# Optimization experiments

Measured on AMD Instinct MI355X. Metric: run time of the kernel, lower is better.

The kernel has to match this reference:

```python
import jax, jax.numpy as jnp
import numpy as np

N_NODES = 100000


def setup_inputs() -> dict:
    key = jax.random.key(0)
    k1, k2, k3, k4, k5 = jax.random.split(key, 5)
    feat = jax.random.normal(k1, (N_NODES, 128), dtype=jnp.float32)
    src = jax.random.randint(k2, (1600000,), 0, N_NODES, dtype=jnp.int32)
    dst = jax.random.randint(k3, (1600000,), 0, N_NODES, dtype=jnp.int32)
    # Xavier-uniform-like weight init
    limit = float(np.sqrt(6.0 / (128 + 128)))
    weight = jax.random.uniform(k4, (128, 128), minval=-limit, maxval=limit, dtype=jnp.float32)
    bias = jax.random.normal(k5, (128,), dtype=jnp.float32) * 0.0  # zeros per reset_parameters
    return {"feat": feat, "src": src, "dst": dst, "weight": weight, "bias": bias}


def reference(feat, src, dst, weight, bias):
    # copy_u/sum: gather source features along edges, scatter-add into destinations
    agg = jax.ops.segment_sum(feat[src], dst, num_segments=N_NODES)  # [N, in_feats]
    rst = agg @ weight  # [N, out_feats]
    # symmetric-ish degree normalization: in_degree^{-0.5}, clamped at 1
    deg = jax.ops.segment_sum(jnp.ones_like(dst, dtype=feat.dtype), dst, num_segments=N_NODES)
    norm = jnp.clip(deg, 1.0, None) ** -0.5  # [N]
    rst = rst * norm[:, None] + bias
    return rst
```

## Files before the change

kernel.cpp:

```cpp
#include <hip/hip_runtime.h>
#include <hip/hip_bf16.h>

#define CHUNK 1024
#define RR 64
#define DEPTH 64
#define WMAX 1600
typedef unsigned int uint;
typedef unsigned short ushort;

typedef __bf16 bf16x8 __attribute__((ext_vector_type(8)));
typedef float  f32x4  __attribute__((ext_vector_type(4)));

__device__ __forceinline__ ushort f2bf(float f) {
    const uint u = __float_as_uint(f);
    return (ushort)((u + 0x7fffu + ((u >> 16) & 1u)) >> 16);
}

__global__ __launch_bounds__(256) void partition64(const int* __restrict__ src,
                                                   const int* __restrict__ dst,
                                                   int* __restrict__ gcur,
                                                   int2* __restrict__ staging,
                                                   int cap, int nE, int N) {
    __shared__ int2 bins[RR][DEPTH];
    __shared__ int cnt[RR];
    __shared__ int res[RR];
    const int t  = threadIdx.x;
    const int nb = gridDim.x;
    const int rounds = (nE + nb * 1024 - 1) / (nb * 1024);

    for (int rd = 0; rd < rounds; ++rd) {
        if (t < RR) cnt[t] = 0;
        __syncthreads();

        const int e4 = (rd * nb + blockIdx.x) * 1024 + t * 4;
        int s[4], d[4];
        int nv = 0;
        if (e4 + 3 < nE) {
            const int4 s4 = *reinterpret_cast<const int4*>(src + e4);
            const int4 d4 = *reinterpret_cast<const int4*>(dst + e4);
            s[0] = s4.x; s[1] = s4.y; s[2] = s4.z; s[3] = s4.w;
            d[0] = d4.x; d[1] = d4.y; d[2] = d4.z; d[3] = d4.w;
            nv = 4;
        } else {
            for (int e = e4; e < nE; ++e) { s[nv] = src[e]; d[nv] = dst[e]; ++nv; }
        }
#pragma unroll
        for (int i = 0; i < 4; ++i) {
            if (i < nv) {
                const int r = (int)(((long long)d[i] * RR) / N);
                const int pos = atomicAdd(&cnt[r], 1);
                if (pos < DEPTH) {
                    bins[r][pos] = make_int2(s[i], d[i]);
                } else {
                    const int gp = atomicAdd(&gcur[r], 1);
                    staging[(size_t)r * cap + gp] = make_int2(s[i], d[i]);
                }
            }
        }
        __syncthreads();
        if (t < RR) {
            int c = cnt[t];
            c = c < DEPTH ? c : DEPTH;
            cnt[t] = c;
            res[t] = (c > 0) ? atomicAdd(&gcur[t], c) : 0;
        }
        __syncthreads();
        {
            const int g = t >> 2;
            const int l = t & 3;
            const int c = cnt[g];
            const int b = res[g];
            for (int i = l; i < c; i += 4)
                staging[(size_t)g * cap + b + i] = bins[g][i];
        }
        __syncthreads();
    }
}

__global__ __launch_bounds__(1024) void range_build(const int2* __restrict__ staging,
                                                    const int* __restrict__ gcur,
                                                    int* __restrict__ deg,
                                                    int* __restrict__ off,
                                                    int* __restrict__ csr,
                                                    int cap, int N) {
    __shared__ int hist[WMAX];
    __shared__ int sbuf[1024];
    __shared__ int sbase;
    const int r = blockIdx.x;
    const int t = threadIdx.x;
    const int lo = (int)(((long long)r * N + RR - 1) / RR);
    const int hi = (int)(((long long)(r + 1) * N + RR - 1) / RR);
    const int W  = hi - lo;
    const int cnt = gcur[r];

    if (t < RR) sbuf[t] = gcur[t];
    for (int i = t; i < W; i += 1024) hist[i] = 0;
    __syncthreads();
    if (t == 0) {
        int b = 0;
        for (int i = 0; i < r; ++i) b += sbuf[i];
        sbase = b;
    }
    const int2* ep = staging + (size_t)r * cap;
    for (int i = t; i < cnt; i += 1024) {
        const int2 p = ep[i];
        atomicAdd(&hist[p.y - lo], 1);
    }
    __syncthreads();
    const int base = sbase;

    const int i0 = t * 2, i1 = t * 2 + 1;
    const int a = (i0 < W) ? hist[i0] : 0;
    const int b = (i1 < W) ? hist[i1] : 0;
    if (i0 < W) deg[lo + i0] = a;
    if (i1 < W) deg[lo + i1] = b;
    const int tsum = a + b;
    sbuf[t] = tsum;
    __syncthreads();
    for (int dd = 1; dd < 1024; dd <<= 1) {
        const int x = (t >= dd) ? sbuf[t - dd] : 0;
        __syncthreads();
        sbuf[t] += x;
        __syncthreads();
    }
    const int excl = sbuf[t] - tsum;
    if (i0 < W) { off[lo + i0] = base + excl;     hist[i0] = base + excl; }
    if (i1 < W) { off[lo + i1] = base + excl + a; hist[i1] = base + excl + a; }
    __syncthreads();

    for (int i = t; i < cnt; i += 1024) {
        const int2 p = ep[i];
        const int pos = atomicAdd(&hist[p.y - lo], 1);
        csr[pos] = p.x;
    }
}

__global__ __launch_bounds__(256) void prep_w(const float* __restrict__ w,
                                              ushort* __restrict__ wt) {
    const int idx = blockIdx.x * 256 + threadIdx.x;
    const int k = idx >> 7;
    const int n = idx & 127;
    wt[n * 128 + k] = f2bf(w[k * 128 + n]);
}

#define APITCH 136
__global__ __launch_bounds__(256, 2) void gemm_mfma(const float* __restrict__ feat,
                                                    const ushort* __restrict__ wt,
                                                    ushort* __restrict__ h, int M) {
    __shared__ ushort A_lds[64 * APITCH];
    const int t    = threadIdx.x;
    const int wave = t >> 6;
    const int lane = t & 63;
    const int quad = lane >> 4;
    const int nn   = lane & 15;
    const int row0 = blockIdx.x * 64;

    union UB { uint4 u; bf16x8 b; };
    UB bfrag[8][4];
#pragma unroll
    for (int ct = 0; ct < 8; ++ct)
#pragma unroll
        for (int kc = 0; kc < 4; ++kc)
            bfrag[ct][kc].u = *reinterpret_cast<const uint4*>(
                wt + (ct * 16 + nn) * 128 + kc * 32 + quad * 8);

#pragma unroll
    for (int p = 0; p < 8; ++p) {
        const int idx = p * 256 + t;
        const int row = idx >> 5;
        const int c4  = (idx & 31) * 4;
        const int grow = row0 + row;
        float4 v = make_float4(0.f, 0.f, 0.f, 0.f);
        if (grow < M)
            v = *reinterpret_cast<const float4*>(&feat[(size_t)grow * 128 + c4]);
        const uint2 pk = make_uint2((uint)f2bf(v.x) | ((uint)f2bf(v.y) << 16),
                                    (uint)f2bf(v.z) | ((uint)f2bf(v.w) << 16));
        *reinterpret_cast<uint2*>(&A_lds[row * APITCH + c4]) = pk;
    }
    __syncthreads();

    union UA { uint4 u; bf16x8 b; };
    UA afrag[4];
#pragma unroll
    for (int kc = 0; kc < 4; ++kc)
        afrag[kc].u = *reinterpret_cast<const uint4*>(
            &A_lds[(wave * 16 + nn) * APITCH + kc * 32 + quad * 8]);

    f32x4 acc[8];
#pragma unroll
    for (int ct = 0; ct < 8; ++ct) {
        acc[ct] = (f32x4){0.f, 0.f, 0.f, 0.f};
#pragma unroll
        for (int kc = 0; kc < 4; ++kc)
            acc[ct] = __builtin_amdgcn_mfma_f32_16x16x32_bf16(
                afrag[kc].b, bfrag[ct][kc].b, acc[ct], 0, 0, 0);
    }
    __syncthreads();

#pragma unroll
    for (int ct = 0; ct < 8; ++ct) {
#pragma unroll
        for (int reg = 0; reg < 4; ++reg) {
            const int rl = wave * 16 + quad * 4 + reg;
            A_lds[rl * APITCH + ct * 16 + nn] = f2bf(acc[ct][reg]);
        }
    }
    __syncthreads();

#pragma unroll
    for (int p = 0; p < 4; ++p) {
        const int idx = p * 256 + t;
        const int row = idx >> 4;
        const int c16 = idx & 15;
        const int grow = row0 + row;
        if (grow < M) {
            const uint4 v = *reinterpret_cast<const uint4*>(&A_lds[row * APITCH + c16 * 8]);
            *reinterpret_cast<uint4*>(&h[(size_t)grow * 128 + c16 * 8]) = v;
        }
    }
}

__global__ __launch_bounds__(256) void aggregate_h(const ushort* __restrict__ h,
                                                   const int* __restrict__ csr,
                                                   const int* __restrict__ off,
                                                   const int* __restrict__ deg,
                                                   const float* __restrict__ bias,
                                                   float* __restrict__ out, int N) {
    const int node = (blockIdx.x * blockDim.x + threadIdx.x) >> 6;
    if (node >= N) return;
    const int lane = threadIdx.x & 63;
    const int q   = lane >> 4;
    const int sub = lane & 15;
    const int start = off[node];
    const int cnt   = deg[node];
    const int end   = start + cnt;

    float acc[8];
#pragma unroll
    for (int k = 0; k < 8; ++k) acc[k] = 0.0f;

#define UNPACK_ADD(rr)                                             \
    do {                                                           \
        acc[0] += __uint_as_float(((rr).x & 0xffffu) << 16);       \
        acc[1] += __uint_as_float((rr).x & 0xffff0000u);           \
        acc[2] += __uint_as_float(((rr).y & 0xffffu) << 16);       \
        acc[3] += __uint_as_float((rr).y & 0xffff0000u);           \
        acc[4] += __uint_as_float(((rr).z & 0xffffu) << 16);       \
        acc[5] += __uint_as_float((rr).z & 0xffff0000u);           \
        acc[6] += __uint_as_float(((rr).w & 0xffffu) << 16);       \
        acc[7] += __uint_as_float((rr).w & 0xffff0000u);           \
    } while (0)

    int j = start;
    for (; j + 15 < end; j += 16) {
        int s[4];
#pragma unroll
        for (int k = 0; k < 4; ++k) s[k] = csr[j + q + 4 * k];
        uint4 r[4];
#pragma unroll
        for (int k = 0; k < 4; ++k)
            r[k] = *reinterpret_cast<const uint4*>(h + (size_t)s[k] * 128 + sub * 8);
#pragma unroll
        for (int k = 0; k < 4; ++k) UNPACK_ADD(r[k]);
    }
    for (; j + 3 < end; j += 4) {
        const int s = csr[j + q];
        const uint4 rr = *reinterpret_cast<const uint4*>(h + (size_t)s * 128 + sub * 8);
        UNPACK_ADD(rr);
    }
    const int rem = end - j;
    if (q < rem) {
        const int s = csr[j + q];
        const uint4 rr = *reinterpret_cast<const uint4*>(h + (size_t)s * 128 + sub * 8);
        UNPACK_ADD(rr);
    }
#undef UNPACK_ADD

#pragma unroll
    for (int k = 0; k < 8; ++k) {
        acc[k] += __shfl_xor(acc[k], 16, 64);
        acc[k] += __shfl_xor(acc[k], 32, 64);
    }

    if (lane < 16) {
        const float nm = rsqrtf(fmaxf((float)cnt, 1.0f));
        const float4 b0 = *reinterpret_cast<const float4*>(bias + sub * 8 + 0);
        const float4 b1 = *reinterpret_cast<const float4*>(bias + sub * 8 + 4);
        float4 o0, o1;
        o0.x = fmaf(acc[0], nm, b0.x);
        o0.y = fmaf(acc[1], nm, b0.y);
        o0.z = fmaf(acc[2], nm, b0.z);
        o0.w = fmaf(acc[3], nm, b0.w);
        o1.x = fmaf(acc[4], nm, b1.x);
        o1.y = fmaf(acc[5], nm, b1.y);
        o1.z = fmaf(acc[6], nm, b1.z);
        o1.w = fmaf(acc[7], nm, b1.w);
        *reinterpret_cast<float4*>(out + (size_t)node * 128 + sub * 8 + 0) = o0;
        *reinterpret_cast<float4*>(out + (size_t)node * 128 + sub * 8 + 4) = o1;
    }
}

__global__ void hist_simple(const int* __restrict__ dst, int* __restrict__ deg, int nE) {
    int e = blockIdx.x * blockDim.x + threadIdx.x;
    if (e < nE) atomicAdd(&deg[dst[e]], 1);
}
__global__ void bucket_simple(const int* __restrict__ src, const int* __restrict__ dst,
                              int* __restrict__ cur, int* __restrict__ csr, int nE) {
    int e = blockIdx.x * blockDim.x + threadIdx.x;
    if (e < nE) {
        int pos = atomicAdd(&cur[dst[e]], 1);
        csr[pos] = src[e];
    }
}
__global__ __launch_bounds__(256) void scan_chunks(const int* __restrict__ deg,
                                                   int* __restrict__ off,
                                                   int* __restrict__ partials, int N) {
    __shared__ int sums[256];
    const int b = blockIdx.x, t = threadIdx.x;
    const int base = b * CHUNK + t * 4;
    int v[4];
#pragma unroll
    for (int i = 0; i < 4; ++i) v[i] = (base + i < N) ? deg[base + i] : 0;
    const int s = v[0] + v[1] + v[2] + v[3];
    sums[t] = s;
    __syncthreads();
    for (int d = 1; d < 256; d <<= 1) {
        int x = (t >= d) ? sums[t - d] : 0;
        __syncthreads();
        sums[t] += x;
        __syncthreads();
    }
    const int excl = sums[t] - s;
    if (t == 255) partials[b] = sums[255];
    int run = excl;
#pragma unroll
    for (int i = 0; i < 4; ++i) {
        if (base + i < N) off[base + i] = run;
        run += v[i];
    }
}
__global__ __launch_bounds__(256) void scan_partials(int* partials, int P) {
    __shared__ int buf[256];
    const int t = threadIdx.x;
    if (P <= 256) {
        const int v = (t < P) ? partials[t] : 0;
        buf[t] = v;
        __syncthreads();
        for (int d = 1; d < 256; d <<= 1) {
            int x = (t >= d) ? buf[t - d] : 0;
            __syncthreads();
            buf[t] += x;
            __syncthreads();
        }
        if (t < P) partials[t] = buf[t] - v;
    } else if (t == 0) {
        int acc = 0;
        for (int i = 0; i < P; ++i) { int v = partials[i]; partials[i] = acc; acc += v; }
    }
}
__global__ void add_base(int* __restrict__ off, int* __restrict__ cur,
                         const int* __restrict__ partials, int N) {
    int i = blockIdx.x * blockDim.x + threadIdx.x;
    if (i < N) {
        int o = off[i] + partials[i >> 10];
        off[i] = o;
        cur[i] = o;
    }
}
__global__ __launch_bounds__(256) void aggregate_f32(const float* __restrict__ feat,
                                                     const int* __restrict__ csr,
                                                     const int* __restrict__ off,
                                                     const int* __restrict__ deg,
                                                     float* __restrict__ out, int N) {
    const int node = (blockIdx.x * blockDim.x + threadIdx.x) >> 6;
    if (node >= N) return;
    const int lane = threadIdx.x & 63;
    const int start = off[node];
    const int end   = start + deg[node];
    const float2* feat2 = reinterpret_cast<const float2*>(feat);
    float ax = 0.0f, ay = 0.0f;
    for (int j = start; j < end; ++j) {
        const float2 v = feat2[(size_t)csr[j] * 64 + lane];
        ax += v.x;
        ay += v.y;
    }
    reinterpret_cast<float2*>(out)[(size_t)node * 64 + lane] = make_float2(ax, ay);
}
__global__ __launch_bounds__(256) void gemm_norm(const float* agg,
                                                 const float* __restrict__ weight,
                                                 const float* __restrict__ bias,
                                                 const int* __restrict__ deg,
                                                 float* out, int M) {
    __shared__ float As[64][68];
    __shared__ float Wc[64][128];
    const int t  = threadIdx.x;
    const int tx = t & 15;
    const int ty = t >> 4;
    const int row0 = blockIdx.x * 64;
    float acc[4][8];
#pragma unroll
    for (int i = 0; i < 4; ++i)
#pragma unroll
        for (int j = 0; j < 8; ++j) acc[i][j] = 0.0f;
    for (int c = 0; c < 2; ++c) {
        if (c) __syncthreads();
        {
            const int k4 = (t & 15) * 4;
            const int rbase = t >> 4;
#pragma unroll
            for (int p = 0; p < 4; ++p) {
                const int rr = rbase + p * 16;
                const int grow = row0 + rr;
                float4 v = make_float4(0.f, 0.f, 0.f, 0.f);
                if (grow < M)
                    v = *reinterpret_cast<const float4*>(&agg[(size_t)grow * 128 + c * 64 + k4]);
                *reinterpret_cast<float4*>(&As[rr][k4]) = v;
            }
        }
        {
#pragma unroll
            for (int p = 0; p < 8; ++p) {
                const int idx = (p * 256 + t) * 4;
                const int kk = idx >> 7;
                const int j = idx & 127;
                *reinterpret_cast<float4*>(&Wc[kk][j]) =
                    *reinterpret_cast<const float4*>(&weight[(c * 64 + kk) * 128 + j]);
            }
        }
        __syncthreads();
#pragma unroll 8
        for (int k = 0; k < 64; ++k) {
            float a[4];
#pragma unroll
            for (int i = 0; i < 4; ++i) a[i] = As[ty * 4 + i][k];
            const float4 b0 = *reinterpret_cast<const float4*>(&Wc[k][tx * 8 + 0]);
            const float4 b1 = *reinterpret_cast<const float4*>(&Wc[k][tx * 8 + 4]);
            const float b[8] = {b0.x, b0.y, b0.z, b0.w, b1.x, b1.y, b1.z, b1.w};
#pragma unroll
            for (int i = 0; i < 4; ++i)
#pragma unroll
                for (int j = 0; j < 8; ++j)
                    acc[i][j] = fmaf(a[i], b[j], acc[i][j]);
        }
    }
    float bcol[8];
#pragma unroll
    for (int j = 0; j < 8; ++j) bcol[j] = bias[tx * 8 + j];
#pragma unroll
    for (int i = 0; i < 4; ++i) {
        const int grow = row0 + ty * 4 + i;
        if (grow < M) {
            const float nm = rsqrtf(fmaxf((float)deg[grow], 1.0f));
            float4 o0, o1;
            o0.x = fmaf(acc[i][0], nm, bcol[0]);
            o0.y = fmaf(acc[i][1], nm, bcol[1]);
            o0.z = fmaf(acc[i][2], nm, bcol[2]);
            o0.w = fmaf(acc[i][3], nm, bcol[3]);
            o1.x = fmaf(acc[i][4], nm, bcol[4]);
            o1.y = fmaf(acc[i][5], nm, bcol[5]);
            o1.z = fmaf(acc[i][6], nm, bcol[6]);
            o1.w = fmaf(acc[i][7], nm, bcol[7]);
            *reinterpret_cast<float4*>(&out[(size_t)grow * 128 + tx * 8 + 0]) = o0;
            *reinterpret_cast<float4*>(&out[(size_t)grow * 128 + tx * 8 + 4]) = o1;
        }
    }
}

extern "C" void kernel_launch(void* const* d_in, const int* in_sizes, int n_in,
                              void* d_out, int out_size, void* d_ws, size_t ws_size,
                              hipStream_t stream) {
    const float* feat   = (const float*)d_in[0];
    const int*   src    = (const int*)d_in[1];
    const int*   dst    = (const int*)d_in[2];
    const float* weight = (const float*)d_in[3];
    const float* bias   = (const float*)d_in[4];
    float* out = (float*)d_out;

    const int nE = in_sizes[1];
    const int M  = in_sizes[0] / 128;
    const int P  = (M + CHUNK - 1) / CHUNK;

    int* degi     = (int*)d_ws;
    int* off      = degi + M;
    int* cur      = off + M;
    int* partials = cur + M;
    int* gcur     = partials + 256;
    int* csr      = gcur + RR;
    ushort* wt    = (ushort*)(csr + nE);
    const size_t wt_end    = ((size_t)3 * M + 256 + RR + (size_t)nE) * sizeof(int) + 32768;
    const size_t stage_off = (wt_end + 15) & ~(size_t)15;
    const int cap = (((nE + RR - 1) / RR + 8192) + 3) & ~3;
    int2* staging = (int2*)((char*)d_ws + stage_off);
    ushort* h     = (ushort*)staging;
    const size_t stage_bytes = (size_t)RR * cap * sizeof(int2);
    const size_t h_bytes     = (size_t)M * 128 * sizeof(ushort);
    const size_t need_big = stage_off + (stage_bytes > h_bytes ? stage_bytes : h_bytes);

    if (ws_size >= need_big) {
        hipMemsetAsync(gcur, 0, RR * sizeof(int), stream);
        prep_w<<<64, 256, 0, stream>>>(weight, wt);
        partition64<<<1024, 256, 0, stream>>>(src, dst, gcur, staging, cap, nE, M);
        range_build<<<RR, 1024, 0, stream>>>(staging, gcur, degi, off, csr, cap, M);
        gemm_mfma<<<(M + 63) / 64, 256, 0, stream>>>(feat, wt, h, M);
        aggregate_h<<<(M + 3) / 4, 256, 0, stream>>>(h, csr, off, degi, bias, out, M);
    } else {
        hipMemsetAsync(degi, 0, (size_t)M * sizeof(int), stream);
        hist_simple<<<(nE + 255) / 256, 256, 0, stream>>>(dst, degi, nE);
        scan_chunks<<<P, 256, 0, stream>>>(degi, off, partials, M);
        scan_partials<<<1, 256, 0, stream>>>(partials, P);
        add_base<<<(M + 255) / 256, 256, 0, stream>>>(off, cur, partials, M);
        bucket_simple<<<(nE + 255) / 256, 256, 0, stream>>>(src, dst, cur, csr, nE);
        aggregate_f32<<<(M + 3) / 4, 256, 0, stream>>>(feat, csr, off, degi, out, M);
        gemm_norm<<<(M + 63) / 64, 256, 0, stream>>>(out, weight, bias, degi, out, M);
    }
}
```

Measured before the change: 249.4 us.

## Fuse CSR build into aggregation with per-block shared-memory sub-range CSR

Packs each edge into 32 bits (17-bit source, local destination offset in the upper bits), halving staging traffic. It removes the range_build kernel and the global deg/off/csr arrays. Each of 1024 blocks filters its range's staging list for its node sub-range, builds a local CSR in shared memory, and aggregates bf16 h rows directly. Each range's staging list is read 16 times, and correctness depends on M fitting in 17 bits and per-block edge counts staying under CAPE (2560). The GEMM is also moved ahead of partitioning.

```diff
diff --git a/kernel.cpp b/kernel.cpp
--- a/kernel.cpp
+++ b/kernel.cpp
@@ -3,8 +3,10 @@
 
 #define CHUNK 1024
 #define RR 64
-#define DEPTH 64
-#define WMAX 1600
+#define PDEPTH 96
+#define NSUB 16
+#define CAPE 2560
+#define SUBWMAX 128
 typedef unsigned int uint;
 typedef unsigned short ushort;
 
@@ -19,9 +21,9 @@
 __global__ __launch_bounds__(256) void partition64(const int* __restrict__ src,
                                                    const int* __restrict__ dst,
                                                    int* __restrict__ gcur,
-                                                   int2* __restrict__ staging,
+                                                   uint* __restrict__ staging,
                                                    int cap, int nE, int N) {
-    __shared__ int2 bins[RR][DEPTH];
+    __shared__ uint bins[RR][PDEPTH];
     __shared__ int cnt[RR];
     __shared__ int res[RR];
     const int t  = threadIdx.x;
@@ -47,91 +49,39 @@
 #pragma unroll
         for (int i = 0; i < 4; ++i) {
             if (i < nv) {
-                const int r = (int)(((long long)d[i] * RR) / N);
+                const int r  = (int)(((long long)d[i] * RR) / N);
+                const int lo = (int)(((long long)r * N + RR - 1) / RR);
+                const uint pk = (uint)s[i] | ((uint)(d[i] - lo) << 17);
                 const int pos = atomicAdd(&cnt[r], 1);
-                if (pos < DEPTH) {
-                    bins[r][pos] = make_int2(s[i], d[i]);
+                if (pos < PDEPTH) {
+                    bins[r][pos] = pk;
                 } else {
                     const int gp = atomicAdd(&gcur[r], 1);
-                    staging[(size_t)r * cap + gp] = make_int2(s[i], d[i]);
+                    staging[(size_t)r * cap + gp] = pk;
                 }
             }
         }
         __syncthreads();
         if (t < RR) {
             int c = cnt[t];
-            c = c < DEPTH ? c : DEPTH;
+            c = c < PDEPTH ? c : PDEPTH;
             cnt[t] = c;
             res[t] = (c > 0) ? atomicAdd(&gcur[t], c) : 0;
         }
         __syncthreads();
         {
-            const int g = t >> 2;
-            const int l = t & 3;
-            const int c = cnt[g];
-            const int b = res[g];
-            for (int i = l; i < c; i += 4)
-                staging[(size_t)g * cap + b + i] = bins[g][i];
-        }
-        __syncthreads();
-    }
-}
-
-__global__ __launch_bounds__(1024) void range_build(const int2* __restrict__ staging,
-                                                    const int* __restrict__ gcur,
-                                                    int* __restrict__ deg,
-                                                    int* __restrict__ off,
-                                                    int* __restrict__ csr,
-                                                    int cap, int N) {
-    __shared__ int hist[WMAX];
-    __shared__ int sbuf[1024];
-    __shared__ int sbase;
-    const int r = blockIdx.x;
-    const int t = threadIdx.x;
-    const int lo = (int)(((long long)r * N + RR - 1) / RR);
-    const int hi = (int)(((long long)(r + 1) * N + RR - 1) / RR);
-    const int W  = hi - lo;
-    const int cnt = gcur[r];
-
-    if (t < RR) sbuf[t] = gcur[t];
-    for (int i = t; i < W; i += 1024) hist[i] = 0;
-    __syncthreads();
-    if (t == 0) {
-        int b = 0;
-        for (int i = 0; i < r; ++i) b += sbuf[i];
-        sbase = b;
-    }
-    const int2* ep = staging + (size_t)r * cap;
-    for (int i = t; i < cnt; i += 1024) {
-        const int2 p = ep[i];
-        atomicAdd(&hist[p.y - lo], 1);
-    }
-    __syncthreads();
-    const int base = sbase;
-
-    const int i0 = t * 2, i1 = t * 2 + 1;
-    const int a = (i0 < W) ? hist[i0] : 0;
-    const int b = (i1 < W) ? hist[i1] : 0;
-    if (i0 < W) deg[lo + i0] = a;
-    if (i1 < W) deg[lo + i1] = b;
-    const int tsum = a + b;
-    sbuf[t] = tsum;
-    __syncthreads();
-    for (int dd = 1; dd < 1024; dd <<= 1) {
-        const int x = (t >= dd) ? sbuf[t - dd] : 0;
-        __syncthreads();
-        sbuf[t] += x;
-        __syncthreads();
-    }
-    const int excl = sbuf[t] - tsum;
-    if (i0 < W) { off[lo + i0] = base + excl;     hist[i0] = base + excl; }
-    if (i1 < W) { off[lo + i1] = base + excl + a; hist[i1] = base + excl + a; }
-    __syncthreads();
-
-    for (int i = t; i < cnt; i += 1024) {
-        const int2 p = ep[i];
-        const int pos = atomicAdd(&hist[p.y - lo], 1);
-        csr[pos] = p.x;
+            const int w    = t >> 6;
+            const int lane = t & 63;
+            for (int rr = w * 16; rr < w * 16 + 16; ++rr) {
+                const int c = cnt[rr];
+                const int b = res[rr];
+                if (lane < c)
+                    staging[(size_t)rr * cap + b + lane] = bins[rr][lane];
+                if (c > 64 && lane + 64 < c)
+                    staging[(size_t)rr * cap + b + 64 + lane] = bins[rr][64 + lane];
+            }
+        }
+        __syncthreads();
     }
 }
 
@@ -220,24 +170,95 @@
     }
 }
 
-__global__ __launch_bounds__(256) void aggregate_h(const ushort* __restrict__ h,
-                                                   const int* __restrict__ csr,
-                                                   const int* __restrict__ off,
-                                                   const int* __restrict__ deg,
-                                                   const float* __restrict__ bias,
-                                                   float* __restrict__ out, int N) {
-    const int node = (blockIdx.x * blockDim.x + threadIdx.x) >> 6;
-    if (node >= N) return;
-    const int lane = threadIdx.x & 63;
+__global__ __launch_bounds__(512, 8) void build_agg(const uint* __restrict__ staging,
+                                                    const int* __restrict__ gcur,
+                                                    const ushort* __restrict__ h,
+                                                    const float* __restrict__ bias,
+                                                    float* __restrict__ out, int cap, int N) {
+    __shared__ uint epack[CAPE];
+    __shared__ int  csr_s[CAPE];
+    __shared__ int  hist[SUBWMAX];
+    __shared__ int  off_s[SUBWMAX];
+    __shared__ int  cur_s[SUBWMAX];
+    __shared__ int  sbuf[SUBWMAX];
+    __shared__ int  scnt;
+
+    const int t    = threadIdx.x;
+    const int bid  = blockIdx.x;
+    const int xcd  = bid & 7;
+    const int i2   = bid >> 3;
+    const int r    = xcd * 8 + (i2 >> 4);
+    const int sub  = i2 & (NSUB - 1);
+
+    const int lo   = (int)(((long long)r * N + RR - 1) / RR);
+    const int hi   = (int)(((long long)(r + 1) * N + RR - 1) / RR);
+    const int W    = hi - lo;
+    const int SUBW = (W + NSUB - 1) / NSUB;
+    const int nlo  = sub * SUBW;
+    const int nhi  = min(W, nlo + SUBW);
+    const int SW   = nhi - nlo;
+    if (SW <= 0) return;
+
+    const int  cnt_r = gcur[r];
+    const uint* ep   = staging + (size_t)r * cap;
+    const int  lane  = t & 63;
+
+    if (t == 0) scnt = 0;
+    if (t < SUBWMAX) hist[t] = 0;
+    __syncthreads();
+
+    const int nall = (cnt_r + 511) & ~511;
+    for (int i = t; i < nall; i += 512) {
+        uint v = 0;
+        bool keep = false;
+        if (i < cnt_r) {
+            v = ep[i];
+            const int ld = (int)(v >> 17);
+            keep = (ld >= nlo) && (ld < nhi);
+        }
+        const unsigned long long m = __ballot(keep);
+        const int tot = __popcll(m);
+        if (tot) {
+            int wb = 0;
+            if (lane == 0) wb = atomicAdd(&scnt, tot);
+            wb = __shfl(wb, 0);
+            if (keep) {
+                const int p = wb + __popcll(m & ((1ull << lane) - 1ull));
+                if (p < CAPE) epack[p] = v;
+            }
+        }
+    }
+    __syncthreads();
+    const int ne = min(scnt, CAPE);
+
+    for (int i = t; i < ne; i += 512)
+        atomicAdd(&hist[(int)(epack[i] >> 17) - nlo], 1);
+    __syncthreads();
+
+    int v0 = 0;
+    if (t < SUBWMAX) { v0 = hist[t]; sbuf[t] = v0; }
+    __syncthreads();
+    for (int d = 1; d < SUBWMAX; d <<= 1) {
+        int x = 0;
+        if (t < SUBWMAX && t >= d) x = sbuf[t - d];
+        __syncthreads();
+        if (t < SUBWMAX) sbuf[t] += x;
+        __syncthreads();
+    }
+    if (t < SUBWMAX) { const int e = sbuf[t] - v0; off_s[t] = e; cur_s[t] = e; }
+    __syncthreads();
+
+    for (int i = t; i < ne; i += 512) {
+        const uint v  = epack[i];
+        const int ld  = (int)(v >> 17) - nlo;
+        const int pos = atomicAdd(&cur_s[ld], 1);
+        csr_s[pos] = (int)(v & 0x1FFFFu);
+    }
+    __syncthreads();
+
+    const int wv  = t >> 6;
     const int q   = lane >> 4;
-    const int sub = lane & 15;
-    const int start = off[node];
-    const int cnt   = deg[node];
-    const int end   = start + cnt;
-
-    float acc[8];
-#pragma unroll
-    for (int k = 0; k < 8; ++k) acc[k] = 0.0f;
+    const int sbl = lane & 15;
 
 #define UNPACK_ADD(rr)                                             \
     do {                                                           \
@@ -251,53 +272,64 @@
         acc[7] += __uint_as_float((rr).w & 0xffff0000u);           \
     } while (0)
 
-    int j = start;
-    for (; j + 15 < end; j += 16) {
-        int s[4];
-#pragma unroll
-        for (int k = 0; k < 4; ++k) s[k] = csr[j + q + 4 * k];
-        uint4 r[4];
-#pragma unroll
-        for (int k = 0; k < 4; ++k)
-            r[k] = *reinterpret_cast<const uint4*>(h + (size_t)s[k] * 128 + sub * 8);
-#pragma unroll
-        for (int k = 0; k < 4; ++k) UNPACK_ADD(r[k]);
-    }
-    for (; j + 3 < end; j += 4) {
-        const int s = csr[j + q];
-        const uint4 rr = *reinterpret_cast<const uint4*>(h + (size_t)s * 128 + sub * 8);
-        UNPACK_ADD(rr);
-    }
-    const int rem = end - j;
-    if (q < rem) {
-        const int s = csr[j + q];
-        const uint4 rr = *reinterpret_cast<const uint4*>(h + (size_t)s * 128 + sub * 8);
-        UNPACK_ADD(rr);
+    for (int n = wv; n < SW; n += 8) {
+        const int start = off_s[n];
+        const int dg    = hist[n];
+        const int end   = start + dg;
+
+        float acc[8];
+#pragma unroll
+        for (int k = 0; k < 8; ++k) acc[k] = 0.0f;
+
+        int j = start;
+        for (; j + 15 < end; j += 16) {
+            int s[4];
+#pragma unroll
+            for (int k = 0; k < 4; ++k) s[k] = csr_s[j + q + 4 * k];
+            uint4 rg[4];
+#pragma unroll
+            for (int k = 0; k < 4; ++k)
+                rg[k] = *reinterpret_cast<const uint4*>(h + (size_t)s[k] * 128 + sbl * 8);
+#pragma unroll
+            for (int k = 0; k < 4; ++k) UNPACK_ADD(rg[k]);
+        }
+        for (; j + 3 < end; j += 4) {
+            const int s = csr_s[j + q];
+            const uint4 rr = *reinterpret_cast<const uint4*>(h + (size_t)s * 128 + sbl * 8);
+            UNPACK_ADD(rr);
+        }
+        const int rem = end - j;
+        if (q < rem) {
+            const int s = csr_s[j + q];
+            const uint4 rr = *reinterpret_cast<const uint4*>(h + (size_t)s * 128 + sbl * 8);
+            UNPACK_ADD(rr);
+        }
+
+#pragma unroll
+        for (int k = 0; k < 8; ++k) {
+            acc[k] += __shfl_xor(acc[k], 16, 64);
+            acc[k] += __shfl_xor(acc[k], 32, 64);
+        }
+
+        if (lane < 16) {
+            const float nm = rsqrtf(fmaxf((float)dg, 1.0f));
+            const float4 b0 = *reinterpret_cast<const float4*>(bias + sbl * 8 + 0);
+            const float4 b1 = *reinterpret_cast<const float4*>(bias + sbl * 8 + 4);
+            float4 o0, o1;
+            o0.x = fmaf(acc[0], nm, b0.x);
+            o0.y = fmaf(acc[1], nm, b0.y);
+            o0.z = fmaf(acc[2], nm, b0.z);
+            o0.w = fmaf(acc[3], nm, b0.w);
+            o1.x = fmaf(acc[4], nm, b1.x);
+            o1.y = fmaf(acc[5], nm, b1.y);
+            o1.z = fmaf(acc[6], nm, b1.z);
+            o1.w = fmaf(acc[7], nm, b1.w);
+            const size_t gnode = (size_t)(lo + nlo + n);
+            *reinterpret_cast<float4*>(out + gnode * 128 + sbl * 8 + 0) = o0;
+            *reinterpret_cast<float4*>(out + gnode * 128 + sbl * 8 + 4) = o1;
+        }
     }
 #undef UNPACK_ADD
-
-#pragma unroll
-    for (int k = 0; k < 8; ++k) {
-        acc[k] += __shfl_xor(acc[k], 16, 64);
-        acc[k] += __shfl_xor(acc[k], 32, 64);
-    }
-
-    if (lane < 16) {
-        const float nm = rsqrtf(fmaxf((float)cnt, 1.0f));
-        const float4 b0 = *reinterpret_cast<const float4*>(bias + sub * 8 + 0);
-        const float4 b1 = *reinterpret_cast<const float4*>(bias + sub * 8 + 4);
-        float4 o0, o1;
-        o0.x = fmaf(acc[0], nm, b0.x);
-        o0.y = fmaf(acc[1], nm, b0.y);
-        o0.z = fmaf(acc[2], nm, b0.z);
-        o0.w = fmaf(acc[3], nm, b0.w);
-        o1.x = fmaf(acc[4], nm, b1.x);
-        o1.y = fmaf(acc[5], nm, b1.y);
-        o1.z = fmaf(acc[6], nm, b1.z);
-        o1.w = fmaf(acc[7], nm, b1.w);
-        *reinterpret_cast<float4*>(out + (size_t)node * 128 + sub * 8 + 0) = o0;
-        *reinterpret_cast<float4*>(out + (size_t)node * 128 + sub * 8 + 4) = o1;
-    }
 }
 
 __global__ void hist_simple(const int* __restrict__ dst, int* __restrict__ deg, int nE) {
@@ -480,30 +512,25 @@
     const int M  = in_sizes[0] / 128;
     const int P  = (M + CHUNK - 1) / CHUNK;
 
-    int* degi     = (int*)d_ws;
-    int* off      = degi + M;
-    int* cur      = off + M;
-    int* partials = cur + M;
-    int* gcur     = partials + 256;
-    int* csr      = gcur + RR;
-    ushort* wt    = (ushort*)(csr + nE);
-    const size_t wt_end    = ((size_t)3 * M + 256 + RR + (size_t)nE) * sizeof(int) + 32768;
-    const size_t stage_off = (wt_end + 15) & ~(size_t)15;
+    int*    gcur    = (int*)d_ws;
+    ushort* wt      = (ushort*)(gcur + RR);
+    uint*   staging = (uint*)(wt + 16384);
     const int cap = (((nE + RR - 1) / RR + 8192) + 3) & ~3;
-    int2* staging = (int2*)((char*)d_ws + stage_off);
-    ushort* h     = (ushort*)staging;
-    const size_t stage_bytes = (size_t)RR * cap * sizeof(int2);
-    const size_t h_bytes     = (size_t)M * 128 * sizeof(ushort);
-    const size_t need_big = stage_off + (stage_bytes > h_bytes ? stage_bytes : h_bytes);
-
-    if (ws_size >= need_big) {
+    ushort* h = (ushort*)(staging + (size_t)RR * cap);
+    const size_t need = (size_t)RR * 4 + 32768 + (size_t)RR * cap * 4 + (size_t)M * 128 * 2;
+
+    if (ws_size >= need && M <= 131072) {
         hipMemsetAsync(gcur, 0, RR * sizeof(int), stream);
         prep_w<<<64, 256, 0, stream>>>(weight, wt);
+        gemm_mfma<<<(M + 63) / 64, 256, 0, stream>>>(feat, wt, h, M);
         partition64<<<1024, 256, 0, stream>>>(src, dst, gcur, staging, cap, nE, M);
-        range_build<<<RR, 1024, 0, stream>>>(staging, gcur, degi, off, csr, cap, M);
-        gemm_mfma<<<(M + 63) / 64, 256, 0, stream>>>(feat, wt, h, M);
-        aggregate_h<<<(M + 3) / 4, 256, 0, stream>>>(h, csr, off, degi, bias, out, M);
+        build_agg<<<RR * NSUB, 512, 0, stream>>>(staging, gcur, h, bias, out, cap, M);
     } else {
+        int* degi     = (int*)d_ws;
+        int* off      = degi + M;
+        int* cur      = off + M;
+        int* partials = cur + M;
+        int* csr      = partials + 256;
         hipMemsetAsync(degi, 0, (size_t)M * sizeof(int), stream);
         hist_simple<<<(nE + 255) / 256, 256, 0, stream>>>(dst, degi, nE);
         scan_chunks<<<P, 256, 0, stream>>>(degi, off, partials, M);
```

Result: no change. 249.3 us (-0.0%).
